# Kernel tuning notes

Hardware: AMD Instinct MI355X
Metric: run time of the kernel (lower is better)

Reference implementation:

```python
import jax, jax.numpy as jnp
import numpy as np

B, DT, DV, DA = 32768, 768, 512, 384
P, HID, HEADS = 128, 256, 4
HD = P // HEADS
EPS = 1e-5


def _proj_block(x, W, b, lnw, lnb):
    # Linear -> LayerNorm -> ReLU (Dropout is identity in eval)
    h = x @ W.T + b
    mu = jnp.mean(h, axis=-1, keepdims=True)
    var = jnp.var(h, axis=-1, keepdims=True)
    h = lnw * (h - mu) * jax.lax.rsqrt(var + EPS) + lnb
    return jax.nn.relu(h)


def _mha1(q, kv, Wqkv, bqkv, Wo, bo):
    # torch.nn.MultiheadAttention with seq_len=1 for both query and key/value.
    Wq, Wk, Wv = jnp.split(Wqkv, 3, axis=0)
    bq, bk, bv = jnp.split(bqkv, 3, axis=0)
    qp = (q @ Wq.T + bq).reshape(-1, HEADS, HD)   # [B,H,hd]
    kp = (kv @ Wk.T + bk).reshape(-1, HEADS, HD)
    vp = (kv @ Wv.T + bv).reshape(-1, HEADS, HD)
    scores = jnp.einsum('bhd,bhd->bh', qp, kp) * np.float32(1.0 / np.sqrt(HD))
    attn = jax.nn.softmax(scores[..., None], axis=-1)  # single key -> ones
    ctx = (attn * vp).reshape(-1, P)
    return ctx @ Wo.T + bo


def _forward(xt, xv, xa,
             Wt, bt, lnw_t, lnb_t,
             Wv_, bv_, lnw_v, lnb_v,
             Wa, ba, lnw_a, lnb_a,
             W_qkv, b_qkv, W_o, b_o,
             Wg, bg, Wf1, bf1, Wf2, bf2, Wout, bout):
    t = _proj_block(xt, Wt, bt, lnw_t, lnb_t)   # [B,P]
    v = _proj_block(xv, Wv_, bv_, lnw_v, lnb_v)
    a = _proj_block(xa, Wa, ba, lnw_a, lnb_a)
    # branch order: tv, ta, vt, va, at, av
    Qs = jnp.stack([t, t, v, v, a, a])          # [6,B,P]
    KVs = jnp.stack([v, a, t, a, t, v])
    ctx = jax.vmap(_mha1)(Qs, KVs, W_qkv, b_qkv, W_o, b_o)  # [6,B,P]
    ctx_b = jnp.transpose(ctx, (1, 0, 2))       # [B,6,P]
    feats = ctx_b.reshape(-1, 6 * P)
    g = jax.nn.softmax(feats @ Wg.T + bg, axis=-1)          # [B,6]
    gated = (ctx_b * g[:, :, None]).reshape(-1, 6 * P)
    h = jax.nn.relu(gated @ Wf1.T + bf1)
    h = jax.nn.relu(h @ Wf2.T + bf2)
    return h @ Wout.T + bout                    # [B,2]


def setup_inputs() -> dict:
    key = jax.random.key(0)
    ks = jax.random.split(key, 16)
    f32 = jnp.float32
    def n(k, shape, s=0.02):
        return jax.random.normal(k, shape, f32) * s
    return {
        'xt': jax.random.normal(ks[0], (B, DT), f32),
        'xv': jax.random.normal(ks[1], (B, DV), f32),
        'xa': jax.random.normal(ks[2], (B, DA), f32),
        'Wt': n(ks[3], (P, DT)), 'bt': jnp.zeros(P, f32),
        'lnw_t': jnp.ones(P, f32), 'lnb_t': jnp.zeros(P, f32),
        'Wv_': n(ks[4], (P, DV)), 'bv_': jnp.zeros(P, f32),
        'lnw_v': jnp.ones(P, f32), 'lnb_v': jnp.zeros(P, f32),
        'Wa': n(ks[5], (P, DA)), 'ba': jnp.zeros(P, f32),
        'lnw_a': jnp.ones(P, f32), 'lnb_a': jnp.zeros(P, f32),
        'W_qkv': n(ks[6], (6, 3 * P, P)), 'b_qkv': jnp.zeros((6, 3 * P), f32),
        'W_o': n(ks[7], (6, P, P)), 'b_o': jnp.zeros((6, P), f32),
        'Wg': n(ks[8], (6, 6 * P)), 'bg': jnp.zeros(6, f32),
        'Wf1': n(ks[9], (HID, 6 * P)), 'bf1': jnp.zeros(HID, f32),
        'Wf2': n(ks[10], (HID, HID)), 'bf2': jnp.zeros(HID, f32),
        'Wout': n(ks[11], (2, HID)), 'bout': jnp.zeros(2, f32),
    }


def reference(xt, xv, xa, Wt, bt, lnw_t, lnb_t, Wv_, bv_, lnw_v, lnb_v,
              Wa, ba, lnw_a, lnb_a, W_qkv, b_qkv, W_o, b_o,
              Wg, bg, Wf1, bf1, Wf2, bf2, Wout, bout):
    return _forward(xt, xv, xa, Wt, bt, lnw_t, lnb_t, Wv_, bv_, lnw_v, lnb_v,
                    Wa, ba, lnw_a, lnb_a, W_qkv, b_qkv, W_o, b_o,
                    Wg, bg, Wf1, bf1, Wf2, bf2, Wout, bout)
```

## Files before the change

### kernel.cpp

```cpp
#include <hip/hip_runtime.h>
#include <math.h>

#define DI __device__ __forceinline__

namespace {

constexpr int PB = 32768;

typedef _Float16 half_t;
typedef float f32x4 __attribute__((ext_vector_type(4)));
typedef _Float16 f16x8 __attribute__((ext_vector_type(8)));

#define MFMA16 __builtin_amdgcn_mfma_f32_16x16x32_f16

DI void gl16(const void* g, void* l) {
  __builtin_amdgcn_global_load_lds((const __attribute__((address_space(1))) void*)g,
                                   (__attribute__((address_space(3))) void*)l, 16, 0, 0);
}
DI f16x8 asH(f32x4 v) { return __builtin_bit_cast(f16x8, v); }

DI size_t fragIdx1(int c, int k, int P) {
  return (size_t)((k >> 5)*(P >> 4) + (c >> 4))*512
       + ((k >> 3) & 3)*128 + (c & 15)*8 + (k & 7);
}


__global__ void k_weff(const float* __restrict__ Wqkv, const float* __restrict__ bqkv,
                       const float* __restrict__ Wo, const float* __restrict__ bo,
                       float* __restrict__ M, float* __restrict__ beff)
{
  const int i = blockIdx.x >> 7;
  const int c = blockIdx.x & 127;
  const int k = threadIdx.x;
  const float* wo_row = Wo + (size_t)(i*128 + c)*128;
  const float* wv = Wqkv + (size_t)(i*384 + 256)*128;
  float acc = 0.f;
#pragma unroll 4
  for (int j = 0; j < 128; ++j)
    acc = fmaf(wo_row[j], wv[j*128 + k], acc);
  M[(size_t)(i*128 + c)*128 + k] = acc;

  __shared__ float red[128];
  const float* bv = bqkv + i*384 + 256;
  red[k] = wo_row[k] * bv[k];
  __syncthreads();
  for (int s = 64; s > 0; s >>= 1) {
    if (k < s) red[k] += red[k + s];
    __syncthreads();
  }
  if (k == 0) beff[i*128 + c] = red[0] + bo[i*128 + c];
}

__global__ void k_nbig2(const float* __restrict__ Wf1, const float* __restrict__ M,
                        const float* __restrict__ beff, half_t* __restrict__ Nf)
{
  const int i = blockIdx.x >> 8;
  const int c = blockIdx.x & 255;
  const int k = threadIdx.x;
  const float* w_row = Wf1 + (size_t)c*768 + i*128;
  const float* Mi = M + (size_t)i*128*128;
  float acc = 0.f;
#pragma unroll 4
  for (int j = 0; j < 128; ++j)
    acc = fmaf(w_row[j], Mi[j*128 + k], acc);
  Nf[fragIdx1(c, i*128 + k, 256)] = (half_t)(acc * 4096.f);

  __shared__ float red[128];
  red[k] = w_row[k] * beff[i*128 + k];
  __syncthreads();
  for (int s = 64; s > 0; s >>= 1) {
    if (k < s) red[k] += red[k + s];
    __syncthreads();
  }
  if (k == 0)
    Nf[fragIdx1(c, 768 + i, 256)] = (half_t)(red[0] * 4096.f);
  if (i == 0 && k < 26)
    Nf[fragIdx1(c, 774 + k, 256)] = (half_t)0.f;
}

__global__ void k_ghat(const float* __restrict__ M, const float* __restrict__ Wg,
                       float* __restrict__ Ghat)
{
  const int j = blockIdx.x / 3;
  const int src = blockIdx.x % 3;
  const int k = threadIdx.x;
  int i0, i1;
  if (src == 0)      { i0 = 2; i1 = 4; }
  else if (src == 1) { i0 = 0; i1 = 5; }
  else               { i0 = 1; i1 = 3; }
  float acc = 0.f;
  for (int t = 0; t < 2; ++t) {
    const int i = t ? i1 : i0;
    const float* Mi = M + (size_t)i*128*128;
    const float* wg = Wg + j*768 + i*128;
#pragma unroll 4
    for (int c = 0; c < 128; ++c)
      acc = fmaf(Mi[c*128 + k], wg[c], acc);
  }
  Ghat[j*384 + src*128 + k] = acc;
}

__global__ void k_svec(const float* __restrict__ beff, const float* __restrict__ Wg,
                       const float* __restrict__ bg, float* __restrict__ svec)
{
  const int j = blockIdx.x;
  const int c = threadIdx.x;
  float p = 0.f;
#pragma unroll
  for (int i = 0; i < 6; ++i)
    p = fmaf(beff[i*128 + c], Wg[j*768 + i*128 + c], p);
  __shared__ float red[128];
  red[c] = p;
  __syncthreads();
  for (int s = 64; s > 0; s >>= 1) {
    if (c < s) red[c] += red[c + s];
    __syncthreads();
  }
  if (c == 0) svec[j] = red[0] + bg[j];
}

__global__ void k_splitf(const float* __restrict__ in, half_t* __restrict__ outb,
                         float scale, int P, int KD)
{
  const int idx = blockIdx.x*256 + threadIdx.x;
  if (idx >= P*KD) return;
  const int c = idx / KD, k = idx - c*KD;
  outb[fragIdx1(c, k, P)] = (half_t)(in[idx] * scale);
}

template<int KD>
DI void proj_body(const float* __restrict__ X, const half_t* __restrict__ BF,
                  const float* __restrict__ bias,
                  const float* __restrict__ lnw, const float* __restrict__ lnb,
                  const float* __restrict__ Ghat, float* __restrict__ tva,
                  float* __restrict__ zpart, int row0, int colOff, int srcIdx,
                  f32x4* Bs)
{
  const int tid = threadIdx.x;
  const int lane = tid & 63, wid = tid >> 6;
  const int l15 = lane & 15, l4 = lane >> 4;
  constexpr int NT = KD >> 5;
  constexpr int NPH = NT >> 2;
  const int r0 = row0 + wid*32;

  const float* xr0 = X + (size_t)(r0 + l15)*KD + l4*8;
  const float* xr1 = X + (size_t)(r0 + 16 + l15)*KD + l4*8;

  f32x4 a0[4], a1[4];
  auto LA = [&](int t, f32x4 (&a)[4]) {
    const int tc = (t < NT) ? t : NT - 1;
    const f32x4* p0 = reinterpret_cast<const f32x4*>(xr0 + tc*32);
    const f32x4* p1 = reinterpret_cast<const f32x4*>(xr1 + tc*32);
    a[0] = p0[0]; a[1] = p0[1]; a[2] = p1[0]; a[3] = p1[1];
  };
  auto SPLIT = [&](f32x4 (&a)[4], f16x8& h0, f16x8& l0, f16x8& h1, f16x8& l1) {
#pragma unroll
    for (int j = 0; j < 4; ++j) {
      half_t x;
      x = (half_t)a[0][j]; h0[j]   = x; l0[j]   = (half_t)(a[0][j] - (float)x);
      x = (half_t)a[1][j]; h0[j+4] = x; l0[j+4] = (half_t)(a[1][j] - (float)x);
      x = (half_t)a[2][j]; h1[j]   = x; l1[j]   = (half_t)(a[2][j] - (float)x);
      x = (half_t)a[3][j]; h1[j+4] = x; l1[j+4] = (half_t)(a[3][j] - (float)x);
    }
  };

  f32x4 acc[2][8];
#pragma unroll
  for (int rg = 0; rg < 2; ++rg)
#pragma unroll
    for (int fn = 0; fn < 8; ++fn) acc[rg][fn] = f32x4{0.f, 0.f, 0.f, 0.f};

  LA(0, a0); LA(1, a1);

  for (int q = 0; q < NPH; ++q) {
    __syncthreads();
    const half_t* s = BF + (size_t)q*16384;
#pragma unroll
    for (int i = 0; i < 8; ++i)
      gl16(s + i*2048 + tid*8, (char*)Bs + i*4096 + wid*1024);
    __syncthreads();
#pragma unroll
    for (int p = 0; p < 4; ++p) {
      const int t = q*4 + p;
      f16x8 h0, l0, h1, l1;
      if (p & 1) { SPLIT(a1, h0, l0, h1, l1); LA(t + 2, a1); }
      else       { SPLIT(a0, h0, l0, h1, l1); LA(t + 2, a0); }
#pragma unroll
      for (int fn = 0; fn < 8; ++fn) {
        f16x8 b = asH(Bs[(p*8 + fn)*64 + lane]);
        acc[0][fn] = MFMA16(h0, b, acc[0][fn], 0, 0, 0);
        acc[0][fn] = MFMA16(l0, b, acc[0][fn], 0, 0, 0);
        acc[1][fn] = MFMA16(h1, b, acc[1][fn], 0, 0, 0);
        acc[1][fn] = MFMA16(l1, b, acc[1][fn], 0, 0, 0);
      }
    }
  }

  float bc[8], lw[8], lb[8], gh[6][8];
#pragma unroll
  for (int fn = 0; fn < 8; ++fn) {
    const int c = fn*16 + l15;
    bc[fn] = bias[c]; lw[fn] = lnw[c]; lb[fn] = lnb[c];
#pragma unroll
    for (int j = 0; j < 6; ++j) gh[j][fn] = Ghat[j*384 + colOff + c];
  }
#pragma unroll
  for (int rg = 0; rg < 2; ++rg) {
#pragma unroll
    for (int r = 0; r < 4; ++r) {
      float h[8];
      float s = 0.f, q2 = 0.f;
#pragma unroll
      for (int fn = 0; fn < 8; ++fn) {
        h[fn] = acc[rg][fn][r]*(1.f/256.f) + bc[fn];
        s += h[fn]; q2 = fmaf(h[fn], h[fn], q2);
      }
#pragma unroll
      for (int m = 1; m <= 8; m <<= 1) { s += __shfl_xor(s, m); q2 += __shfl_xor(q2, m); }
      const float mean = s*(1.f/128.f);
      const float var  = q2*(1.f/128.f) - mean*mean;
      const float rstd = rsqrtf(var + 1e-5f);
      float o[8];
#pragma unroll
      for (int fn = 0; fn < 8; ++fn)
        o[fn] = fmaxf(fmaf((h[fn] - mean)*rstd, lw[fn], lb[fn]), 0.f);
      const int grow = r0 + rg*16 + l4*4 + r;
      float* tp = tva + (size_t)grow*384 + colOff;
#pragma unroll
      for (int fn = 0; fn < 8; ++fn) tp[fn*16 + l15] = o[fn];
      float s6[6];
#pragma unroll
      for (int j = 0; j < 6; ++j) {
        float z = 0.f;
#pragma unroll
        for (int fn = 0; fn < 8; ++fn) z = fmaf(o[fn], gh[j][fn], z);
#pragma unroll
        for (int m = 1; m <= 8; m <<= 1) z += __shfl_xor(z, m);
        s6[j] = z;
      }
#pragma unroll
      for (int j = 0; j < 6; ++j)
        if (l15 == j) zpart[(size_t)(srcIdx*PB + grow)*6 + j] = s6[j];
    }
  }
}

__global__ __launch_bounds__(256, 3)
void k_proj(const float* __restrict__ xt, const float* __restrict__ xv,
            const float* __restrict__ xa, const half_t* __restrict__ Wft,
            const half_t* __restrict__ Wfv, const half_t* __restrict__ Wfa,
            const float* __restrict__ bt, const float* __restrict__ lnwt, const float* __restrict__ lnbt,
            const float* __restrict__ bvp, const float* __restrict__ lnwv, const float* __restrict__ lnbv,
            const float* __restrict__ bap, const float* __restrict__ lnwa, const float* __restrict__ lnba,
            const float* __restrict__ Ghat, float* __restrict__ tva, float* __restrict__ zpart)
{
  __shared__ f32x4 Bs[2048];
  const int src = blockIdx.y;
  const int row0 = blockIdx.x * 128;
  if (src == 0)
    proj_body<768>(xt, Wft, bt, lnwt, lnbt, Ghat, tva, zpart, row0, 0, 0, Bs);
  else if (src == 1)
    proj_body<512>(xv, Wfv, bvp, lnwv, lnbv, Ghat, tva, zpart, row0, 128, 1, Bs);
  else
    proj_body<384>(xa, Wfa, bap, lnwa, lnba, Ghat, tva, zpart, row0, 256, 2, Bs);
}

__global__ void k_gate2(const float* __restrict__ zp, const float* __restrict__ svec,
                        float* __restrict__ g)
{
  const int r = blockIdx.x*256 + threadIdx.x;
  float z[6];
#pragma unroll
  for (int j = 0; j < 6; ++j)
    z[j] = zp[(size_t)r*6 + j] + zp[(size_t)(PB + r)*6 + j] + zp[(size_t)(2*PB + r)*6 + j] + svec[j];
  float mx = z[0];
#pragma unroll
  for (int j = 1; j < 6; ++j) mx = fmaxf(mx, z[j]);
  float e[6], s = 0.f;
#pragma unroll
  for (int j = 0; j < 6; ++j) { e[j] = expf(z[j] - mx); s += e[j]; }
  const float inv = 1.f / s;
#pragma unroll
  for (int j = 0; j < 6; ++j) g[(size_t)r*6 + j] = e[j]*inv;
}

__global__ __launch_bounds__(256, 3)
void k_f1(const float* __restrict__ tva, const half_t* __restrict__ Nf,
          const float* __restrict__ gbuf, const float* __restrict__ bias,
          half_t* __restrict__ h1h)
{
  __shared__ f32x4 Bs[2048];
  const int tid = threadIdx.x;
  const int row0 = blockIdx.x * 128;
  const int colOff = blockIdx.y * 128;
  const int fn0 = colOff >> 4;
  const int lane = tid & 63, wid = tid >> 6;
  const int l15 = lane & 15, l4 = lane >> 4;
  const int r0 = row0 + wid*32;

  const float* ar0 = tva + (size_t)(r0 + l15)*384 + l4*8;
  const float* ar1 = tva + (size_t)(r0 + 16 + l15)*384 + l4*8;

  f32x4 a0[4], a1[4];
  auto LA = [&](int t, f32x4 (&a)[4]) {
    const int tc = (t < 24) ? t : 23;
    const int koff = ((0x102021 >> ((tc >> 2)*4)) & 3)*128 + (tc & 3)*32;
    const f32x4* p0 = reinterpret_cast<const f32x4*>(ar0 + koff);
    const f32x4* p1 = reinterpret_cast<const f32x4*>(ar1 + koff);
    a[0] = p0[0]; a[1] = p0[1]; a[2] = p1[0]; a[3] = p1[1];
  };
  auto SPLITG = [&](f32x4 (&a)[4], float s0, float s1,
                    f16x8& h0, f16x8& l0, f16x8& h1, f16x8& l1) {
#pragma unroll
    for (int j = 0; j < 4; ++j) {
      float v; half_t x;
      v = a[0][j]*s0; x = (half_t)v; h0[j]   = x; l0[j]   = (half_t)(v - (float)x);
      v = a[1][j]*s0; x = (half_t)v; h0[j+4] = x; l0[j+4] = (half_t)(v - (float)x);
      v = a[2][j]*s1; x = (half_t)v; h1[j]   = x; l1[j]   = (half_t)(v - (float)x);
      v = a[3][j]*s1; x = (half_t)v; h1[j+4] = x; l1[j+4] = (half_t)(v - (float)x);
    }
  };

  f32x4 acc[2][8];
#pragma unroll
  for (int rg = 0; rg < 2; ++rg)
#pragma unroll
    for (int fn = 0; fn < 8; ++fn) acc[rg][fn] = f32x4{0.f, 0.f, 0.f, 0.f};

  LA(0, a0); LA(1, a1);

  for (int q = 0; q < 6; ++q) {
    const float sq0 = gbuf[(size_t)(r0 + l15)*6 + q] * 16.f;
    const float sq1 = gbuf[(size_t)(r0 + 16 + l15)*6 + q] * 16.f;
    __syncthreads();
#pragma unroll
    for (int p = 0; p < 4; ++p) {
      const half_t* sp = Nf + ((size_t)(q*4 + p)*16 + fn0)*512;
#pragma unroll
      for (int i = 0; i < 2; ++i)
        gl16(sp + i*2048 + tid*8, (char*)Bs + p*8192 + i*4096 + wid*1024);
    }
    __syncthreads();
#pragma unroll
    for (int p = 0; p < 4; ++p) {
      const int t = q*4 + p;
      f16x8 h0, l0, h1, l1;
      if (p & 1) { SPLITG(a1, sq0, sq1, h0, l0, h1, l1); LA(t + 2, a1); }
      else       { SPLITG(a0, sq0, sq1, h0, l0, h1, l1); LA(t + 2, a0); }
#pragma unroll
      for (int fn = 0; fn < 8; ++fn) {
        f16x8 b = asH(Bs[(p*8 + fn)*64 + lane]);
        acc[0][fn] = MFMA16(h0, b, acc[0][fn], 0, 0, 0);
        acc[0][fn] = MFMA16(l0, b, acc[0][fn], 0, 0, 0);
        acc[1][fn] = MFMA16(h1, b, acc[1][fn], 0, 0, 0);
        acc[1][fn] = MFMA16(l1, b, acc[1][fn], 0, 0, 0);
      }
    }
  }

  __syncthreads();
  {
    const half_t* sT = Nf + ((size_t)24*16 + fn0)*512;
#pragma unroll
    for (int i = 0; i < 2; ++i)
      gl16(sT + i*2048 + tid*8, (char*)Bs + i*4096 + wid*1024);
  }
  __syncthreads();
  {
    f16x8 h0, h1;
#pragma unroll
    for (int j = 0; j < 8; ++j) {
      h0[j] = (l4 == 0 && j < 6) ? (half_t)(gbuf[(size_t)(r0 + l15)*6 + j]*16.f) : (half_t)0.f;
      h1[j] = (l4 == 0 && j < 6) ? (half_t)(gbuf[(size_t)(r0 + 16 + l15)*6 + j]*16.f) : (half_t)0.f;
    }
#pragma unroll
    for (int fn = 0; fn < 8; ++fn) {
      f16x8 b = asH(Bs[fn*64 + lane]);
      acc[0][fn] = MFMA16(h0, b, acc[0][fn], 0, 0, 0);
      acc[1][fn] = MFMA16(h1, b, acc[1][fn], 0, 0, 0);
    }
  }

  float bc[8];
#pragma unroll
  for (int fn = 0; fn < 8; ++fn) bc[fn] = bias[colOff + fn*16 + l15];
#pragma unroll
  for (int rg = 0; rg < 2; ++rg)
#pragma unroll
    for (int fn = 0; fn < 8; ++fn)
#pragma unroll
      for (int r = 0; r < 4; ++r) {
        float v = acc[rg][fn][r]*(1.f/65536.f) + bc[fn];
        v = fmaxf(v, 0.f) * 256.f;
        const int grow = r0 + rg*16 + l4*4 + r;
        h1h[(size_t)grow*256 + colOff + fn*16 + l15] = (half_t)v;
      }
}

__global__ __launch_bounds__(256, 3)
void k_f2(const half_t* __restrict__ h1h, const half_t* __restrict__ WF,
          const float* __restrict__ bias, const float* __restrict__ Wout,
          float* __restrict__ part)
{
  __shared__ f32x4 Bs[2048];
  const int tid = threadIdx.x;
  const int row0 = blockIdx.x * 128;
  const int colOff = blockIdx.y * 128;
  const int fn0 = colOff >> 4;
  const int lane = tid & 63, wid = tid >> 6;
  const int l15 = lane & 15, l4 = lane >> 4;
  const int r0 = row0 + wid*32;

  const half_t* hr0 = h1h + (size_t)(r0 + l15)*256 + l4*8;
  const half_t* hr1 = h1h + (size_t)(r0 + 16 + l15)*256 + l4*8;

  f16x8 a0[2], a1[2];
  auto LA = [&](int t, f16x8 (&a)[2]) {
    const int tc = (t < 8) ? t : 7;
    a[0] = *reinterpret_cast<const f16x8*>(hr0 + tc*32);
    a[1] = *reinterpret_cast<const f16x8*>(hr1 + tc*32);
  };

  f32x4 acc[2][8];
#pragma unroll
  for (int rg = 0; rg < 2; ++rg)
#pragma unroll
    for (int fn = 0; fn < 8; ++fn) acc[rg][fn] = f32x4{0.f, 0.f, 0.f, 0.f};

  LA(0, a0); LA(1, a1);

  for (int q = 0; q < 2; ++q) {
    __syncthreads();
#pragma unroll
    for (int p = 0; p < 4; ++p) {
      const half_t* sp = WF + ((size_t)(q*4 + p)*16 + fn0)*512;
#pragma unroll
      for (int i = 0; i < 2; ++i)
        gl16(sp + i*2048 + tid*8, (char*)Bs + p*8192 + i*4096 + wid*1024);
    }
    __syncthreads();
#pragma unroll
    for (int p = 0; p < 4; ++p) {
      const int t = q*4 + p;
      f16x8 h0, h1;
      if (p & 1) { h0 = a1[0]; h1 = a1[1]; LA(t + 2, a1); }
      else       { h0 = a0[0]; h1 = a0[1]; LA(t + 2, a0); }
#pragma unroll
      for (int fn = 0; fn < 8; ++fn) {
        f16x8 b = asH(Bs[(p*8 + fn)*64 + lane]);
        acc[0][fn] = MFMA16(h0, b, acc[0][fn], 0, 0, 0);
        acc[1][fn] = MFMA16(h1, b, acc[1][fn], 0, 0, 0);
      }
    }
  }

  float bc[8], w0[8], w1[8];
#pragma unroll
  for (int fn = 0; fn < 8; ++fn) {
    const int c = colOff + fn*16 + l15;
    bc[fn] = bias[c]; w0[fn] = Wout[c]; w1[fn] = Wout[256 + c];
  }
#pragma unroll
  for (int rg = 0; rg < 2; ++rg)
#pragma unroll
    for (int r = 0; r < 4; ++r) {
      float s0 = 0.f, s1 = 0.f;
#pragma unroll
      for (int fn = 0; fn < 8; ++fn) {
        float hv = fmaxf(acc[rg][fn][r]*(1.f/65536.f) + bc[fn], 0.f);
        s0 = fmaf(hv, w0[fn], s0);
        s1 = fmaf(hv, w1[fn], s1);
      }
#pragma unroll
      for (int m = 1; m <= 8; m <<= 1) { s0 += __shfl_xor(s0, m); s1 += __shfl_xor(s1, m); }
      if (l15 == rg*4 + r) {
        const int grow = r0 + rg*16 + l4*4 + r;
        float* pp = part + ((size_t)blockIdx.y*PB + grow)*2;
        pp[0] = s0; pp[1] = s1;
      }
    }
}

__global__ void k_comb(const float* __restrict__ part, const float* __restrict__ bout,
                       float* __restrict__ out)
{
  const int id = blockIdx.x*256 + threadIdx.x;
  const int j = id & 1;
  float s = bout[j];
#pragma unroll
  for (int s2 = 0; s2 < 2; ++s2) s += part[(size_t)s2*PB*2 + id];
  out[id] = s;
}

}

extern "C" void kernel_launch(void* const* d_in, const int* in_sizes, int n_in,
                              void* d_out, int out_size, void* d_ws, size_t ws_size,
                              hipStream_t stream)
{
  const float* xt   = (const float*)d_in[0];
  const float* xv   = (const float*)d_in[1];
  const float* xa   = (const float*)d_in[2];
  const float* Wt   = (const float*)d_in[3];
  const float* bt   = (const float*)d_in[4];
  const float* lnwt = (const float*)d_in[5];
  const float* lnbt = (const float*)d_in[6];
  const float* Wv   = (const float*)d_in[7];
  const float* bv   = (const float*)d_in[8];
  const float* lnwv = (const float*)d_in[9];
  const float* lnbv = (const float*)d_in[10];
  const float* Wa   = (const float*)d_in[11];
  const float* ba   = (const float*)d_in[12];
  const float* lnwa = (const float*)d_in[13];
  const float* lnba = (const float*)d_in[14];
  const float* Wqkv = (const float*)d_in[15];
  const float* bqkv = (const float*)d_in[16];
  const float* Wo   = (const float*)d_in[17];
  const float* bo   = (const float*)d_in[18];
  const float* Wg   = (const float*)d_in[19];
  const float* bg   = (const float*)d_in[20];
  const float* Wf1  = (const float*)d_in[21];
  const float* bf1  = (const float*)d_in[22];
  const float* Wf2  = (const float*)d_in[23];
  const float* bf2  = (const float*)d_in[24];
  const float* Woutp= (const float*)d_in[25];
  const float* boutp= (const float*)d_in[26];
  float* out = (float*)d_out;

  float* ws   = (float*)d_ws;
  float* tva  = ws;
  float* g    = tva  + (size_t)PB*384;
  float* h1pf = g    + (size_t)PB*6;
  float* M    = h1pf + (size_t)PB*128;
  float* beff = M    + 98304;
  half_t* Wft = (half_t*)(beff + 768);
  half_t* Wfv = Wft + 98304;
  half_t* Wfa = Wfv + 65536;
  half_t* Nf  = Wfa + 49152;
  half_t* WF2 = Nf + 204800;
  float* Ghat = (float*)(WF2 + 65536);
  float* svec = Ghat + 2304;
  half_t* h1h = (half_t*)h1pf;
  float* zpart = h1pf;
  float* part  = tva;

  k_weff<<<768, 128, 0, stream>>>(Wqkv, bqkv, Wo, bo, M, beff);
  k_nbig2<<<1536, 128, 0, stream>>>(Wf1, M, beff, Nf);
  k_ghat<<<18, 128, 0, stream>>>(M, Wg, Ghat);
  k_svec<<<6, 128, 0, stream>>>(beff, Wg, bg, svec);
  k_splitf<<<(128*768 + 255)/256, 256, 0, stream>>>(Wt, Wft, 256.f, 128, 768);
  k_splitf<<<(128*512 + 255)/256, 256, 0, stream>>>(Wv, Wfv, 256.f, 128, 512);
  k_splitf<<<(128*384 + 255)/256, 256, 0, stream>>>(Wa, Wfa, 256.f, 128, 384);
  k_splitf<<<(256*256 + 255)/256, 256, 0, stream>>>(Wf2, WF2, 256.f, 256, 256);

  k_proj<<<dim3(256, 3), 256, 0, stream>>>(xt, xv, xa, Wft, Wfv, Wfa,
                                           bt, lnwt, lnbt, bv, lnwv, lnbv, ba, lnwa, lnba,
                                           Ghat, tva, zpart);

  k_gate2<<<PB/256, 256, 0, stream>>>(zpart, svec, g);

  k_f1<<<dim3(256, 2), 256, 0, stream>>>(tva, Nf, g, bf1, h1h);
  k_f2<<<dim3(256, 2), 256, 0, stream>>>(h1h, WF2, bf2, Woutp, part);
  k_comb<<<256, 256, 0, stream>>>(part, boutp, out);
}
```

Before: 176.1 us.

## Stage activation tiles into LDS via async global_load_lds with XOR swizzle

The projection kernel now loads the fp32 X activation tiles straight into shared memory with global_load_lds, using an XOR swizzle to avoid bank conflicts. This replaces the per-thread register prefetch of two K-steps. The K loop now advances 64 columns per phase instead of 128, and the B tile buffer is halved so the new A buffer fits. The aim is coalesced asynchronous loads and lower register pressure. The cost is no overlap between loads and MFMA inside a phase, since each phase does load, sync, compute, and there are twice as many barriers.

```diff
diff --git a/kernel.cpp b/kernel.cpp
--- a/kernel.cpp
+++ b/kernel.cpp
@@ -134,60 +134,60 @@
                   const float* __restrict__ lnw, const float* __restrict__ lnb,
                   const float* __restrict__ Ghat, float* __restrict__ tva,
                   float* __restrict__ zpart, int row0, int colOff, int srcIdx,
-                  f32x4* Bs)
+                  f32x4* As, f32x4* Bs)
 {
   const int tid = threadIdx.x;
   const int lane = tid & 63, wid = tid >> 6;
   const int l15 = lane & 15, l4 = lane >> 4;
-  constexpr int NT = KD >> 5;
-  constexpr int NPH = NT >> 2;
+  constexpr int NPH = KD >> 6;
   const int r0 = row0 + wid*32;
 
-  const float* xr0 = X + (size_t)(r0 + l15)*KD + l4*8;
-  const float* xr1 = X + (size_t)(r0 + 16 + l15)*KD + l4*8;
-
-  f32x4 a0[4], a1[4];
-  auto LA = [&](int t, f32x4 (&a)[4]) {
-    const int tc = (t < NT) ? t : NT - 1;
-    const f32x4* p0 = reinterpret_cast<const f32x4*>(xr0 + tc*32);
-    const f32x4* p1 = reinterpret_cast<const f32x4*>(xr1 + tc*32);
-    a[0] = p0[0]; a[1] = p0[1]; a[2] = p1[0]; a[3] = p1[1];
-  };
-  auto SPLIT = [&](f32x4 (&a)[4], f16x8& h0, f16x8& l0, f16x8& h1, f16x8& l1) {
-#pragma unroll
-    for (int j = 0; j < 4; ++j) {
-      half_t x;
-      x = (half_t)a[0][j]; h0[j]   = x; l0[j]   = (half_t)(a[0][j] - (float)x);
-      x = (half_t)a[1][j]; h0[j+4] = x; l0[j+4] = (half_t)(a[1][j] - (float)x);
-      x = (half_t)a[2][j]; h1[j]   = x; l1[j]   = (half_t)(a[2][j] - (float)x);
-      x = (half_t)a[3][j]; h1[j+4] = x; l1[j+4] = (half_t)(a[3][j] - (float)x);
-    }
-  };
-
   f32x4 acc[2][8];
 #pragma unroll
   for (int rg = 0; rg < 2; ++rg)
 #pragma unroll
     for (int fn = 0; fn < 8; ++fn) acc[rg][fn] = f32x4{0.f, 0.f, 0.f, 0.f};
 
-  LA(0, a0); LA(1, a1);
-
   for (int q = 0; q < NPH; ++q) {
     __syncthreads();
-    const half_t* s = BF + (size_t)q*16384;
-#pragma unroll
-    for (int i = 0; i < 8; ++i)
-      gl16(s + i*2048 + tid*8, (char*)Bs + i*4096 + wid*1024);
-    __syncthreads();
-#pragma unroll
-    for (int p = 0; p < 4; ++p) {
-      const int t = q*4 + p;
+#pragma unroll
+    for (int i = 0; i < 8; ++i) {
+      const int row_l = wid*32 + i*4 + (lane >> 4);
+      const char* src = (const char*)X + (size_t)(row0 + row_l)*KD*4 + q*256
+                      + (((lane & 15)*16) ^ ((row_l & 7) << 5));
+      gl16(src, (char*)As + wid*8192 + i*1024);
+    }
+    {
+      const half_t* s = BF + (size_t)q*8192;
+#pragma unroll
+      for (int i = 0; i < 4; ++i)
+        gl16(s + i*2048 + tid*8, (char*)Bs + i*4096 + wid*1024);
+    }
+    __syncthreads();
+#pragma unroll
+    for (int tb = 0; tb < 2; ++tb) {
       f16x8 h0, l0, h1, l1;
-      if (p & 1) { SPLIT(a1, h0, l0, h1, l1); LA(t + 2, a1); }
-      else       { SPLIT(a0, h0, l0, h1, l1); LA(t + 2, a0); }
+#pragma unroll
+      for (int rg = 0; rg < 2; ++rg) {
+        const int row_l = wid*32 + rg*16 + l15;
+        const int off = row_l*256 + ((tb*128 + l4*32) ^ ((row_l & 7) << 5));
+        f32x4 v0 = *reinterpret_cast<const f32x4*>((const char*)As + off);
+        f32x4 v1 = *reinterpret_cast<const f32x4*>((const char*)As + off + 16);
+#pragma unroll
+        for (int j = 0; j < 4; ++j) {
+          half_t x;
+          if (rg == 0) {
+            x = (half_t)v0[j]; h0[j]   = x; l0[j]   = (half_t)(v0[j] - (float)x);
+            x = (half_t)v1[j]; h0[j+4] = x; l0[j+4] = (half_t)(v1[j] - (float)x);
+          } else {
+            x = (half_t)v0[j]; h1[j]   = x; l1[j]   = (half_t)(v0[j] - (float)x);
+            x = (half_t)v1[j]; h1[j+4] = x; l1[j+4] = (half_t)(v1[j] - (float)x);
+          }
+        }
+      }
 #pragma unroll
       for (int fn = 0; fn < 8; ++fn) {
-        f16x8 b = asH(Bs[(p*8 + fn)*64 + lane]);
+        f16x8 b = asH(Bs[(tb*8 + fn)*64 + lane]);
         acc[0][fn] = MFMA16(h0, b, acc[0][fn], 0, 0, 0);
         acc[0][fn] = MFMA16(l0, b, acc[0][fn], 0, 0, 0);
         acc[1][fn] = MFMA16(h1, b, acc[1][fn], 0, 0, 0);
@@ -254,15 +254,16 @@
             const float* __restrict__ bap, const float* __restrict__ lnwa, const float* __restrict__ lnba,
             const float* __restrict__ Ghat, float* __restrict__ tva, float* __restrict__ zpart)
 {
-  __shared__ f32x4 Bs[2048];
+  __shared__ f32x4 As[2048];
+  __shared__ f32x4 Bs[1024];
   const int src = blockIdx.y;
   const int row0 = blockIdx.x * 128;
   if (src == 0)
-    proj_body<768>(xt, Wft, bt, lnwt, lnbt, Ghat, tva, zpart, row0, 0, 0, Bs);
+    proj_body<768>(xt, Wft, bt, lnwt, lnbt, Ghat, tva, zpart, row0, 0, 0, As, Bs);
   else if (src == 1)
-    proj_body<512>(xv, Wfv, bvp, lnwv, lnbv, Ghat, tva, zpart, row0, 128, 1, Bs);
+    proj_body<512>(xv, Wfv, bvp, lnwv, lnbv, Ghat, tva, zpart, row0, 128, 1, As, Bs);
   else
-    proj_body<384>(xa, Wfa, bap, lnwa, lnba, Ghat, tva, zpart, row0, 256, 2, Bs);
+    proj_body<384>(xa, Wfa, bap, lnwa, lnba, Ghat, tva, zpart, row0, 256, 2, As, Bs);
 }
 
 __global__ void k_gate2(const float* __restrict__ zp, const float* __restrict__ svec,
```

After: 171.6 us. -2.6%, faster.
